# Performance work log

Measured on AMD Instinct MI355X. Metric: run time of the kernel, lower is better.

The kernel has to match this reference:

```python
import jax, jax.numpy as jnp
import numpy as np

B, H, SQ, SKV, D = 2, 16, 2048, 2048, 64
SCALE = 8  # sqrt(head_dim)


def setup_inputs() -> dict:
    key = jax.random.key(0)
    kq, kk, kv, km = jax.random.split(key, 4)
    q = jax.random.normal(kq, (B, H, SQ, D), dtype=jnp.float32)
    k = jax.random.normal(kk, (B, H, SKV, D), dtype=jnp.float32)
    v = jax.random.normal(kv, (B, H, SKV, D), dtype=jnp.float32)
    mask = jax.random.normal(km, (1, 1, SQ, SKV), dtype=jnp.float32)
    return {"q": q, "k": k, "v": v, "mask": mask, "scale": SCALE}


def reference(q, k, v, mask, scale):
    # scores: [B, H, SQ, SKV]
    scores = jnp.einsum("bhqd,bhkd->bhqk", q, k) / scale
    scores = scores + mask  # broadcast additive mask
    probs = jax.nn.softmax(scores, axis=-1)
    # hidden: [B, H, SQ, D]
    return jnp.einsum("bhqk,bhkd->bhqd", probs, v)
```

## Files before the change

### kernel.cpp

```cpp
#include <hip/hip_runtime.h>
#include <hip/hip_bf16.h>

#define NB 2
#define NH 16
#define NSQ 2048
#define NSKV 2048
#define ND 64
#define NT (NSKV / 64)
#define LOG2E 1.4426950408889634f
#define BHSTRIDE (NSKV * ND)

typedef __attribute__((ext_vector_type(8))) short bf16x8;
typedef __attribute__((ext_vector_type(4))) float f32x4;
typedef __attribute__((address_space(1))) const unsigned gas_u32;
typedef __attribute__((address_space(3))) unsigned las_u32;

__device__ __forceinline__ short f2bf(float x) {
  union { float f; unsigned u; } c; c.f = x;
  unsigned r = c.u + 0x7fffu + ((c.u >> 16) & 1u);
  return (short)(r >> 16);
}
__device__ __forceinline__ unsigned pack_bf2(float lo, float hi) {
  union { __hip_bfloat162 h; unsigned u; } c;
  c.h = __float22bfloat162_rn(float2{lo, hi});
  return c.u;
}
__device__ __forceinline__ float u2f(unsigned u) {
  union { unsigned u; float f; } c; c.u = u; return c.f;
}
__device__ __forceinline__ float exp2_fast(float x) {
#if __has_builtin(__builtin_amdgcn_exp2f)
  return __builtin_amdgcn_exp2f(x);
#else
  return exp2f(x);
#endif
}

__device__ __forceinline__ int kvmap(int x) {
  return (x & 3) | (((x >> 4) & 1) << 2) | (((x >> 2) & 1) << 3)
       | (((x >> 3) & 1) << 4) | (x & 32);
}

__global__ void prep_all(const float* __restrict__ K, const float* __restrict__ V,
                         const float* __restrict__ M, short* __restrict__ Kp,
                         short* __restrict__ Vp, unsigned short* __restrict__ Mt) {
  __shared__ float T[64][65];
  const int tile = blockIdx.x;
  const int bh   = blockIdx.y;
  const int kv0  = tile * 64;
  const int t    = (int)threadIdx.x;

  {
    const float* src = V + ((size_t)bh * NSKV + kv0) * ND;
#pragma unroll
    for (int i = 0; i < 4; ++i) {
      float4 v = *(const float4*)(src + (size_t)((t >> 4) + 16 * i) * ND + (t & 15) * 4);
      T[(t >> 4) + 16 * i][(t & 15) * 4 + 0] = v.x;
      T[(t >> 4) + 16 * i][(t & 15) * 4 + 1] = v.y;
      T[(t >> 4) + 16 * i][(t & 15) * 4 + 2] = v.z;
      T[(t >> 4) + 16 * i][(t & 15) * 4 + 3] = v.w;
    }
    __syncthreads();
    const int d = t >> 2, c = t & 3;
    bf16x8 w0, w1;
#pragma unroll
    for (int j = 0; j < 8; ++j) w0[j] = f2bf(T[c * 16 + j][d]);
#pragma unroll
    for (int j = 0; j < 8; ++j) w1[j] = f2bf(T[c * 16 + 8 + j][d]);
    const int frag  = (d >> 4) * 2 + (c >> 1);
    const int lane0 = (((2 * c) & 3) << 4) | (d & 15);
    const int lane1 = (((2 * c + 1) & 3) << 4) | (d & 15);
    short* dstb = Vp + (size_t)bh * BHSTRIDE + (size_t)tile * 4096 + frag * 512;
    *(bf16x8*)(dstb + lane0 * 8) = w0;
    *(bf16x8*)(dstb + lane1 * 8) = w1;
  }

#pragma unroll
  for (int h = 0; h < 2; ++h) {
    const int u    = t + h * 256;
    const int nt   = u >> 7, kc = (u >> 6) & 1, lane = u & 63;
    const int prow = nt * 16 + (lane & 15);
    const float* src = K + ((size_t)bh * NSKV + kv0 + kvmap(prow)) * ND
                         + kc * 32 + (lane >> 4) * 8;
    float4 a = *(const float4*)src, b = *(const float4*)(src + 4);
    bf16x8 w;
    w[0]=f2bf(a.x); w[1]=f2bf(a.y); w[2]=f2bf(a.z); w[3]=f2bf(a.w);
    w[4]=f2bf(b.x); w[5]=f2bf(b.y); w[6]=f2bf(b.z); w[7]=f2bf(b.w);
    *(bf16x8*)(Kp + (size_t)bh * BHSTRIDE + (size_t)tile * 4096 + u * 8) = w;
  }

  {
    const int rl = t >> 4, c = t & 15;
    const int nt   = 2 * (c >> 3) + (c & 1);
    const int lq   = (c >> 1) & 3;
    const int lane = lq * 16 + rl;
#pragma unroll
    for (int i = 0; i < 4; ++i) {
      const int qt  = bh * 4 + i;
      const int row = qt * 16 + rl;
      float4 v = *(const float4*)(M + (size_t)row * NSKV + tile * 64 + c * 4);
      ushort4 o;
      o.x = (unsigned short)f2bf(LOG2E * v.x);
      o.y = (unsigned short)f2bf(LOG2E * v.y);
      o.z = (unsigned short)f2bf(LOG2E * v.z);
      o.w = (unsigned short)f2bf(LOG2E * v.w);
      *(ushort4*)(Mt + (((size_t)qt * 32 + tile) * 64 + lane) * 16 + nt * 4) = o;
    }
  }
}

__global__ __launch_bounds__(256, 2)
void attn_fwd(const float* __restrict__ Q, const short* __restrict__ Kp,
              const short* __restrict__ Vp, const unsigned short* __restrict__ Mt,
              const void* __restrict__ scale_p, float* __restrict__ O)
{
  const int lin = (int)blockIdx.x + ((int)blockIdx.y << 4);
  const int swz = ((lin & 7) << 6) | (lin >> 3);
  const int qb  = swz & 15;
  const int bh  = swz >> 4;

  const int tid = (int)threadIdx.x;
  const int wv  = tid >> 6;
  const int ln  = tid & 63;
  const int l16 = ln & 15;
  const int lq  = ln >> 4;

  float scale_v;
  {
    union { int i; float f; } u;
    u.i = ((const int*)scale_p)[0];
    float af = fabsf(u.f);
    scale_v = (af >= 1e-6f && af <= 1e6f) ? u.f : (float)u.i;
  }
  const float qmul = LOG2E / scale_v;

  const int q0 = qb * 128;
  const short* Kb = Kp + (size_t)bh * BHSTRIDE;
  const short* Vb = Vp + (size_t)bh * BHSTRIDE;

  __shared__ short Kl[2][4096];
  __shared__ short Vl[2][4096];

  bf16x8 qf[2][2];
#pragma unroll
  for (int qs = 0; qs < 2; ++qs) {
    const float* qrow = Q + ((size_t)bh * NSQ + q0 + wv * 32 + qs * 16 + l16) * ND;
#pragma unroll
    for (int kc = 0; kc < 2; ++kc) {
      const float4* p = (const float4*)(qrow + kc * 32 + lq * 8);
      float4 a = p[0], b = p[1];
      bf16x8 f;
      f[0]=f2bf(a.x*qmul); f[1]=f2bf(a.y*qmul); f[2]=f2bf(a.z*qmul); f[3]=f2bf(a.w*qmul);
      f[4]=f2bf(b.x*qmul); f[5]=f2bf(b.y*qmul); f[6]=f2bf(b.z*qmul); f[7]=f2bf(b.w*qmul);
      qf[qs][kc] = f;
    }
  }

  f32x4 oa[2][4];
  f32x4 lacc[2];
#pragma unroll
  for (int qs = 0; qs < 2; ++qs) {
#pragma unroll
    for (int dt = 0; dt < 4; ++dt) { f32x4 z = {0.f,0.f,0.f,0.f}; oa[qs][dt] = z; }
    f32x4 z = {0.f,0.f,0.f,0.f}; lacc[qs] = z;
  }

  bf16x8 ones;
#pragma unroll
  for (int j = 0; j < 8; ++j) ones[j] = (short)0x3F80;

  const unsigned short* M0 = Mt + (size_t)(qb * 8 + wv * 2) * 32768 + (size_t)ln * 16;
  const unsigned short* M1 = M0 + 32768;

  auto mload = [&](int t, float4* mf0, float4* mf1) {
    const unsigned short* p0 = M0 + (size_t)t * 1024;
    const unsigned short* p1 = M1 + (size_t)t * 1024;
    uint4 a0 = *(const uint4*)p0, b0 = *(const uint4*)(p0 + 8);
    uint4 a1 = *(const uint4*)p1, b1 = *(const uint4*)(p1 + 8);
    const unsigned u0[8] = {a0.x,a0.y,a0.z,a0.w,b0.x,b0.y,b0.z,b0.w};
    const unsigned u1[8] = {a1.x,a1.y,a1.z,a1.w,b1.x,b1.y,b1.z,b1.w};
#pragma unroll
    for (int nt = 0; nt < 4; ++nt) {
      mf0[nt] = float4{u2f(u0[nt*2] << 16), u2f(u0[nt*2] & 0xffff0000u),
                       u2f(u0[nt*2+1] << 16), u2f(u0[nt*2+1] & 0xffff0000u)};
      mf1[nt] = float4{u2f(u1[nt*2] << 16), u2f(u1[nt*2] & 0xffff0000u),
                       u2f(u1[nt*2+1] << 16), u2f(u1[nt*2+1] & 0xffff0000u)};
    }
  };

  auto stage = [&](int t, int buf) {
    const short* ks = Kb + (size_t)t * 4096;
    const short* vs = Vb + (size_t)t * 4096;
#pragma unroll
    for (int i = 0; i < 2; ++i) {
      const int chunk = wv * 2 + i;
      __builtin_amdgcn_global_load_lds((gas_u32*)(ks + chunk * 512 + ln * 8),
                                       (las_u32*)&Kl[buf][chunk * 512], 16, 0, 0);
      __builtin_amdgcn_global_load_lds((gas_u32*)(vs + chunk * 512 + ln * 8),
                                       (las_u32*)&Vl[buf][chunk * 512], 16, 0, 0);
    }
  };

  auto smpack = [&](f32x4 (&s)[4], bf16x8 (&pa)[2]) {
#pragma unroll
    for (int nt = 0; nt < 4; ++nt) {
      s[nt][0] = exp2_fast(s[nt][0]);
      s[nt][1] = exp2_fast(s[nt][1]);
      s[nt][2] = exp2_fast(s[nt][2]);
      s[nt][3] = exp2_fast(s[nt][3]);
    }
#pragma unroll
    for (int kc = 0; kc < 2; ++kc) {
      union { unsigned u[4]; bf16x8 v; } w;
      w.u[0] = pack_bf2(s[2*kc][0],   s[2*kc][1]);
      w.u[1] = pack_bf2(s[2*kc][2],   s[2*kc][3]);
      w.u[2] = pack_bf2(s[2*kc+1][0], s[2*kc+1][1]);
      w.u[3] = pack_bf2(s[2*kc+1][2], s[2*kc+1][3]);
      pa[kc] = w.v;
    }
  };

  auto tile = [&](int t, int buf, float4 (&mc0)[4], float4 (&mc1)[4],
                  float4 (&mn0)[4], float4 (&mn1)[4]) {
    if (t + 1 < NT) {
      stage(t + 1, buf ^ 1);
      __builtin_amdgcn_sched_barrier(0);
      mload(t + 1, mn0, mn1);
    }
    bf16x8 kf[4][2];
#pragma unroll
    for (int nt = 0; nt < 4; ++nt)
#pragma unroll
      for (int kc = 0; kc < 2; ++kc)
        kf[nt][kc] = *(const bf16x8*)&Kl[buf][(nt * 2 + kc) * 512 + ln * 8];

    f32x4 s0[4], s1[4];
    __builtin_amdgcn_s_setprio(1);
#pragma unroll
    for (int nt = 0; nt < 4; ++nt) {
      f32x4 a = *(const f32x4*)&mc0[nt];
      a = __builtin_amdgcn_mfma_f32_16x16x32_bf16(kf[nt][0], qf[0][0], a, 0, 0, 0);
      a = __builtin_amdgcn_mfma_f32_16x16x32_bf16(kf[nt][1], qf[0][1], a, 0, 0, 0);
      s0[nt] = a;
    }
#pragma unroll
    for (int nt = 0; nt < 4; ++nt) {
      f32x4 a = *(const f32x4*)&mc1[nt];
      a = __builtin_amdgcn_mfma_f32_16x16x32_bf16(kf[nt][0], qf[1][0], a, 0, 0, 0);
      a = __builtin_amdgcn_mfma_f32_16x16x32_bf16(kf[nt][1], qf[1][1], a, 0, 0, 0);
      s1[nt] = a;
    }
    __builtin_amdgcn_s_setprio(0);

    bf16x8 vf[4][2];
#pragma unroll
    for (int dt = 0; dt < 4; ++dt)
#pragma unroll
      for (int kc = 0; kc < 2; ++kc)
        vf[dt][kc] = *(const bf16x8*)&Vl[buf][(dt * 2 + kc) * 512 + ln * 8];

    bf16x8 pa0[2], pa1[2];
    smpack(s0, pa0);

    __builtin_amdgcn_s_setprio(1);
#pragma unroll
    for (int kc = 0; kc < 2; ++kc) {
#pragma unroll
      for (int dt = 0; dt < 4; ++dt)
        oa[0][dt] = __builtin_amdgcn_mfma_f32_16x16x32_bf16(pa0[kc], vf[dt][kc], oa[0][dt], 0, 0, 0);
      lacc[0] = __builtin_amdgcn_mfma_f32_16x16x32_bf16(pa0[kc], ones, lacc[0], 0, 0, 0);
    }
    __builtin_amdgcn_s_setprio(0);

    smpack(s1, pa1);

    __builtin_amdgcn_s_setprio(1);
#pragma unroll
    for (int kc = 0; kc < 2; ++kc) {
#pragma unroll
      for (int dt = 0; dt < 4; ++dt)
        oa[1][dt] = __builtin_amdgcn_mfma_f32_16x16x32_bf16(pa1[kc], vf[dt][kc], oa[1][dt], 0, 0, 0);
      lacc[1] = __builtin_amdgcn_mfma_f32_16x16x32_bf16(pa1[kc], ones, lacc[1], 0, 0, 0);
    }
    __builtin_amdgcn_s_setprio(0);

    __builtin_amdgcn_sched_barrier(0);
    asm volatile("s_waitcnt vmcnt(4)" ::: "memory");
    __builtin_amdgcn_s_barrier();
    __builtin_amdgcn_sched_barrier(0);
  };

  float4 mA0[4], mA1[4], mB0[4], mB1[4];
  stage(0, 0);
  mload(0, mA0, mA1);
  __syncthreads();

  for (int t = 0; t < NT; t += 2) {
    tile(t,     0, mA0, mA1, mB0, mB1);
    tile(t + 1, 1, mB0, mB1, mA0, mA1);
  }

#pragma unroll
  for (int qs = 0; qs < 2; ++qs)
#pragma unroll
    for (int r = 0; r < 4; ++r) {
      const float inv = 1.0f / lacc[qs][r];
      float* orow = O + ((size_t)bh * NSQ + q0 + wv * 32 + qs * 16 + lq * 4 + r) * ND;
#pragma unroll
      for (int dt = 0; dt < 4; ++dt)
        orow[dt * 16 + l16] = oa[qs][dt][r] * inv;
    }
}

extern "C" void kernel_launch(void* const* d_in, const int* in_sizes, int n_in,
                              void* d_out, int out_size, void* d_ws, size_t ws_size,
                              hipStream_t stream) {
  const float* q     = (const float*)d_in[0];
  const float* k     = (const float*)d_in[1];
  const float* v     = (const float*)d_in[2];
  const float* mask  = (const float*)d_in[3];
  const void*  scale = (const void*)d_in[4];
  float* out = (float*)d_out;

  const size_t NELEM = (size_t)NB * NH * NSKV * ND;
  short* Kpk = (short*)d_ws;
  short* Vpk = Kpk + NELEM;
  unsigned short* Mtl = (unsigned short*)(Vpk + NELEM);

  prep_all<<<dim3(NSKV / 64, NB * NH), 256, 0, stream>>>(k, v, mask, Kpk, Vpk, Mtl);

  dim3 grid(NSQ / 128, NB * NH);
  attn_fwd<<<grid, 256, 0, stream>>>(q, Kpk, Vpk, Mtl, scale, out);
}
```

Before: 67.66 us.

## Give each wave private K LDS buffers, load V directly, drop block barriers

Each wave now stages its own copy of the K tile into per-wave LDS buffers, so the per-tile workgroup barrier is removed. V fragments are loaded straight from global memory into registers instead of going through LDS. Mask values stay packed as bf16 words and are expanded just before the MFMA. The intent is to remove barrier stalls and cross-wave coupling, at the cost of four times the K traffic from L2 and four times the LDS footprint. Correctness relies on the hand-written vmcnt counts matching the outstanding loads.

```diff
diff --git a/kernel.cpp b/kernel.cpp
--- a/kernel.cpp
+++ b/kernel.cpp
@@ -138,8 +138,7 @@
   const short* Kb = Kp + (size_t)bh * BHSTRIDE;
   const short* Vb = Vp + (size_t)bh * BHSTRIDE;
 
-  __shared__ short Kl[2][4096];
-  __shared__ short Vl[2][4096];
+  __shared__ short Kw[4][2][4096];
 
   bf16x8 qf[2][2];
 #pragma unroll
@@ -172,33 +171,30 @@
   const unsigned short* M0 = Mt + (size_t)(qb * 8 + wv * 2) * 32768 + (size_t)ln * 16;
   const unsigned short* M1 = M0 + 32768;
 
-  auto mload = [&](int t, float4* mf0, float4* mf1) {
+  union MU { uint4 q[2]; unsigned u[8]; };
+
+  auto mload = [&](int t, MU& m0, MU& m1) {
     const unsigned short* p0 = M0 + (size_t)t * 1024;
     const unsigned short* p1 = M1 + (size_t)t * 1024;
-    uint4 a0 = *(const uint4*)p0, b0 = *(const uint4*)(p0 + 8);
-    uint4 a1 = *(const uint4*)p1, b1 = *(const uint4*)(p1 + 8);
-    const unsigned u0[8] = {a0.x,a0.y,a0.z,a0.w,b0.x,b0.y,b0.z,b0.w};
-    const unsigned u1[8] = {a1.x,a1.y,a1.z,a1.w,b1.x,b1.y,b1.z,b1.w};
-#pragma unroll
-    for (int nt = 0; nt < 4; ++nt) {
-      mf0[nt] = float4{u2f(u0[nt*2] << 16), u2f(u0[nt*2] & 0xffff0000u),
-                       u2f(u0[nt*2+1] << 16), u2f(u0[nt*2+1] & 0xffff0000u)};
-      mf1[nt] = float4{u2f(u1[nt*2] << 16), u2f(u1[nt*2] & 0xffff0000u),
-                       u2f(u1[nt*2+1] << 16), u2f(u1[nt*2+1] & 0xffff0000u)};
-    }
+    m0.q[0] = *(const uint4*)p0;
+    m0.q[1] = *(const uint4*)(p0 + 8);
+    m1.q[0] = *(const uint4*)p1;
+    m1.q[1] = *(const uint4*)(p1 + 8);
   };
 
   auto stage = [&](int t, int buf) {
     const short* ks = Kb + (size_t)t * 4096;
-    const short* vs = Vb + (size_t)t * 4096;
-#pragma unroll
-    for (int i = 0; i < 2; ++i) {
-      const int chunk = wv * 2 + i;
-      __builtin_amdgcn_global_load_lds((gas_u32*)(ks + chunk * 512 + ln * 8),
-                                       (las_u32*)&Kl[buf][chunk * 512], 16, 0, 0);
-      __builtin_amdgcn_global_load_lds((gas_u32*)(vs + chunk * 512 + ln * 8),
-                                       (las_u32*)&Vl[buf][chunk * 512], 16, 0, 0);
-    }
+#pragma unroll
+    for (int c = 0; c < 8; ++c)
+      __builtin_amdgcn_global_load_lds((gas_u32*)(ks + c * 512 + ln * 8),
+                                       (las_u32*)&Kw[wv][buf][c * 512], 16, 0, 0);
+  };
+
+  auto vload = [&](int t, bf16x8 (&vf)[4][2]) {
+    const short* vt = Vb + (size_t)t * 4096 + ln * 8;
+#pragma unroll
+    for (int f = 0; f < 8; ++f)
+      vf[f >> 1][f & 1] = *(const bf16x8*)(vt + f * 512);
   };
 
   auto smpack = [&](f32x4 (&s)[4], bf16x8 (&pa)[2]) {
@@ -220,45 +216,54 @@
     }
   };
 
-  auto tile = [&](int t, int buf, float4 (&mc0)[4], float4 (&mc1)[4],
-                  float4 (&mn0)[4], float4 (&mn1)[4]) {
+  auto tile = [&](int t, int buf, MU& mc0, MU& mc1, MU& mn0, MU& mn1) {
+    bf16x8 vf[4][2];
+    __builtin_amdgcn_sched_barrier(0);
+    vload(t, vf);
+    __builtin_amdgcn_sched_barrier(0);
     if (t + 1 < NT) {
       stage(t + 1, buf ^ 1);
       __builtin_amdgcn_sched_barrier(0);
       mload(t + 1, mn0, mn1);
-    }
+      __builtin_amdgcn_sched_barrier(0);
+      asm volatile("s_waitcnt vmcnt(20)" ::: "memory");
+    } else {
+      __builtin_amdgcn_sched_barrier(0);
+      asm volatile("s_waitcnt vmcnt(8)" ::: "memory");
+    }
+    __builtin_amdgcn_sched_barrier(0);
+
     bf16x8 kf[4][2];
 #pragma unroll
     for (int nt = 0; nt < 4; ++nt)
 #pragma unroll
       for (int kc = 0; kc < 2; ++kc)
-        kf[nt][kc] = *(const bf16x8*)&Kl[buf][(nt * 2 + kc) * 512 + ln * 8];
+        kf[nt][kc] = *(const bf16x8*)&Kw[wv][buf][(nt * 2 + kc) * 512 + ln * 8];
 
     f32x4 s0[4], s1[4];
     __builtin_amdgcn_s_setprio(1);
 #pragma unroll
     for (int nt = 0; nt < 4; ++nt) {
-      f32x4 a = *(const f32x4*)&mc0[nt];
+      const unsigned w0 = mc0.u[nt * 2], w1 = mc0.u[nt * 2 + 1];
+      f32x4 a;
+      a[0] = u2f(w0 << 16); a[1] = u2f(w0 & 0xffff0000u);
+      a[2] = u2f(w1 << 16); a[3] = u2f(w1 & 0xffff0000u);
       a = __builtin_amdgcn_mfma_f32_16x16x32_bf16(kf[nt][0], qf[0][0], a, 0, 0, 0);
       a = __builtin_amdgcn_mfma_f32_16x16x32_bf16(kf[nt][1], qf[0][1], a, 0, 0, 0);
       s0[nt] = a;
     }
 #pragma unroll
     for (int nt = 0; nt < 4; ++nt) {
-      f32x4 a = *(const f32x4*)&mc1[nt];
+      const unsigned w0 = mc1.u[nt * 2], w1 = mc1.u[nt * 2 + 1];
+      f32x4 a;
+      a[0] = u2f(w0 << 16); a[1] = u2f(w0 & 0xffff0000u);
+      a[2] = u2f(w1 << 16); a[3] = u2f(w1 & 0xffff0000u);
       a = __builtin_amdgcn_mfma_f32_16x16x32_bf16(kf[nt][0], qf[1][0], a, 0, 0, 0);
       a = __builtin_amdgcn_mfma_f32_16x16x32_bf16(kf[nt][1], qf[1][1], a, 0, 0, 0);
       s1[nt] = a;
     }
     __builtin_amdgcn_s_setprio(0);
 
-    bf16x8 vf[4][2];
-#pragma unroll
-    for (int dt = 0; dt < 4; ++dt)
-#pragma unroll
-      for (int kc = 0; kc < 2; ++kc)
-        vf[dt][kc] = *(const bf16x8*)&Vl[buf][(dt * 2 + kc) * 512 + ln * 8];
-
     bf16x8 pa0[2], pa1[2];
     smpack(s0, pa0);
 
@@ -283,17 +288,11 @@
       lacc[1] = __builtin_amdgcn_mfma_f32_16x16x32_bf16(pa1[kc], ones, lacc[1], 0, 0, 0);
     }
     __builtin_amdgcn_s_setprio(0);
-
-    __builtin_amdgcn_sched_barrier(0);
-    asm volatile("s_waitcnt vmcnt(4)" ::: "memory");
-    __builtin_amdgcn_s_barrier();
-    __builtin_amdgcn_sched_barrier(0);
-  };
-
-  float4 mA0[4], mA1[4], mB0[4], mB1[4];
+  };
+
+  MU mA0, mA1, mB0, mB1;
   stage(0, 0);
   mload(0, mA0, mA1);
-  __syncthreads();
 
   for (int t = 0; t < NT; t += 2) {
     tile(t,     0, mA0, mA1, mB0, mB1);
```

After: 74.88 us. 10.7% more time.
